# Performance work log

Hardware: AMD Instinct MI355X
Metric: run time of the kernel (lower is better)

## Reference

```python
import jax, jax.numpy as jnp
import numpy as np

PAD, BOS, EOS, UNK = 0, 1, 2, 3
B, S, V, D, L = 256, 512, 50000, 256, 128

def setup_inputs() -> dict:
    key = jax.random.key(0)
    ks = jax.random.split(key, 12)
    vocab_tensor = jax.random.randint(ks[0], (B, S), 4, V)
    parent_idx = jax.random.randint(ks[1], (B, S), 0, S)
    pbond = jax.random.randint(ks[2], (B, S), 0, 4)
    bond = jax.random.randint(ks[3], (B, S), 0, 4)
    patom = jax.random.randint(ks[4], (B, S), 0, 16)
    atom = jax.random.randint(ks[5], (B, S), 0, 16)
    btype = jax.random.randint(ks[6], (B, S), 0, 4)
    order_tensor = jnp.stack([parent_idx, pbond, bond, patom, atom, btype], axis=-1)
    lengths = jax.random.randint(ks[7], (B,), 1, S + 1)
    mask_tensor = jnp.arange(S)[None, :] < lengths[:, None]  # ragged prefix masks
    eps = jax.random.normal(ks[8], (B, L), dtype=jnp.float32)
    sc = 1.0 / np.sqrt(D)
    emb = jax.random.normal(ks[9], (V, D), dtype=jnp.float32) * sc
    Wm = jax.random.normal(ks[10], (D, L), dtype=jnp.float32) * sc
    Wv = jax.random.normal(ks[11], (D, L), dtype=jnp.float32) * sc
    Wlin = jax.random.normal(jax.random.fold_in(key, 20), (L, D), dtype=jnp.float32) / np.sqrt(L)
    Wout = jax.random.normal(jax.random.fold_in(key, 21), (D, D), dtype=jnp.float32) * sc
    return {
        'vocab_tensor': vocab_tensor, 'order_tensor': order_tensor, 'mask_tensor': mask_tensor,
        'eps': eps, 'emb': emb, 'Wm': Wm, 'bm': jnp.zeros((L,), jnp.float32),
        'Wv': Wv, 'bv': jnp.zeros((L,), jnp.float32), 'Wlin': Wlin,
        'blin': jnp.zeros((D,), jnp.float32), 'Wout': Wout, 'bout': jnp.zeros((D,), jnp.float32),
    }

def _forward(vocab_tensor, order_tensor, mask_tensor, eps, emb, Wm, bm, Wv, bv, Wlin, blin, Wout, bout):
    # --- mask bond-pos columns (torch.where assignments, vectorized) ---
    # (columns 1 and 2 set to -1 where masked; kept implicitly via vt/pad handling)
    # --- calc_chem_z path: masked vocab, parent gather, edge one-hot ---
    vt = jnp.where(mask_tensor, vocab_tensor, PAD)                      # [B,S]
    vocab_emb = emb[vt]                                                 # [B,S,D]
    oi = order_tensor[..., 0]
    oi = jnp.where(oi == -1, BOS, oi)
    parent = jnp.where(mask_tensor, jnp.take_along_axis(vt, oi, axis=1), PAD)
    parent = parent.at[:, 0].set(BOS)
    parent_emb = emb[parent]                                            # [B,S,D]
    idx = jnp.clip(order_tensor[..., 5] - 1, -1, None)
    edge_type = jnp.where((idx >= 0)[..., None],
                          jax.nn.one_hot(jnp.clip(idx, 0), 3, dtype=jnp.float32), 0.0)  # [B,S,3]
    # pooling stand-in for (undefined) StructureEncoder -> [B,D]
    m = mask_tensor[..., None].astype(jnp.float32)
    enc = ((vocab_emb + parent_emb) * m).sum(1) / jnp.maximum(m.sum(1), 1.0)
    enc = enc * (1.0 + 0.0 * edge_type.sum())  # keep edge_type in graph
    # --- LatentSampler ---
    mean = enc @ Wm + bm
    log_var = enc @ Wv + bv
    z = mean + eps * jnp.exp(0.5 * log_var)
    memory = z @ Wlin + blin                                            # [B,D]
    # --- vectorized bos/eos/pad sequence assembly (the hot loop in torch) ---
    inp = jnp.concatenate([jnp.full((B, 1), BOS, vocab_tensor.dtype), vocab_tensor], axis=1)  # [B,S+1]
    mask_ex = jnp.concatenate([jnp.ones((B, 1), bool), mask_tensor], axis=1)
    tgt = jnp.roll(inp, -1, axis=1)
    first_false = jnp.argmax(~mask_ex, axis=1)                          # first eos position
    has_false = jnp.any(~mask_ex, axis=1)
    pos = jnp.arange(S + 1)[None, :]
    tgt = jnp.where(has_false[:, None] & (pos == first_false[:, None] - 1), EOS, tgt)
    kill = has_false[:, None] & (pos >= first_false[:, None])
    tgt = jnp.where(kill, PAD, tgt)
    inp = jnp.where(kill, PAD, inp)
    # edge_index assembly (faithful, consumed by decoder in original)
    padneg = jnp.full((B, 1), -1, order_tensor.dtype)
    edge_index = jnp.concatenate([padneg, jnp.where(mask_tensor, order_tensor[..., 0], -2) + 1], axis=1)
    # --- embedding lookups + decoder stand-in + output head ---
    node_embed = emb[inp]                                               # [B,S+1,D]
    dec = node_embed + memory[:, None, :]
    dec = dec + 0.0 * edge_index[..., None].astype(jnp.float32)         # keep edge_index in graph
    word_emb = dec @ Wout + bout
    tgt_emb = emb[tgt]
    valid = (tgt != PAD)
    sq = (word_emb - tgt_emb) ** 2 * valid[..., None]
    token_loss = sq.sum() / jnp.maximum(valid.sum() * D, 1).astype(jnp.float32)
    kl = -0.5 * jnp.sum(1.0 + log_var - mean ** 2 - jnp.exp(log_var)) / B
    return token_loss, kl

def reference(vocab_tensor, order_tensor, mask_tensor, eps, emb, Wm, bm, Wv, bv, Wlin, blin, Wout, bout):
    return _forward(vocab_tensor, order_tensor, mask_tensor, eps, emb, Wm, bm, Wv, bv, Wlin, blin, Wout, bout)
```

## Files before the change

### kernel.cpp

```cpp
#include <hip/hip_runtime.h>

#define B_ 256
#define S_ 512
#define V_ 50000
#define D_ 256
#define L_ 128
#define PGRID 512

typedef __attribute__((ext_vector_type(8))) short short8;
typedef __attribute__((ext_vector_type(4))) float floatx4;

#define OFF_LENS 16
#define OFF_Q    (OFF_LENS + B_)
#define OFF_WT   (OFF_Q + B_ * D_)
#define OFF_SQP  (OFF_WT + 32768)
#define OFF_EB   (OFF_SQP + 256)
#define OFF_P    (OFF_EB + (V_ * D_ / 2))

__device__ __forceinline__ unsigned short f2bf(float x) {
    unsigned u = __float_as_uint(x);
    u += 0x7FFFu + ((u >> 16) & 1u);
    return (unsigned short)(u >> 16);
}
__device__ __forceinline__ float bf2f(unsigned short u) {
    return __uint_as_float(((unsigned)u) << 16);
}

__global__ __launch_bounds__(256) void prep_kernel(const float* __restrict__ emb,
                                                   const float* __restrict__ Wout,
                                                   unsigned short* __restrict__ embb,
                                                   unsigned short* __restrict__ Wt,
                                                   float* __restrict__ ws) {
    __shared__ float sT[64][65];
    const int tid = threadIdx.x;
    if (blockIdx.x == 0) {
        if (tid < 16) ((int*)ws)[tid] = 0;
        ws[OFF_SQP + tid] = 0.f;
    }
    if (blockIdx.x < 16) {
        const int bx = blockIdx.x;
        const int k0 = (bx & 3) * 64, n0 = (bx >> 2) * 64;
        const int c = tid & 63, rg = tid >> 6;
#pragma unroll
        for (int i = 0; i < 16; ++i) {
            int r = rg * 16 + i;
            sT[c][r] = Wout[(k0 + r) * D_ + n0 + c];
        }
        __syncthreads();
#pragma unroll
        for (int i = 0; i < 16; ++i) {
            int r = rg * 16 + i;
            Wt[(size_t)(n0 + r) * D_ + k0 + c] = f2bf(sT[r][c]);
        }
    }
    const int N4 = V_ * D_ / 4;
    for (int i = blockIdx.x * 256 + tid; i < N4; i += gridDim.x * 256) {
        float4 v = ((const float4*)emb)[i];
        ushort4 h;
        h.x = f2bf(v.x); h.y = f2bf(v.y); h.z = f2bf(v.z); h.w = f2bf(v.w);
        ((ushort4*)embb)[i] = h;
    }
}

__global__ __launch_bounds__(1024) void enclat_kernel(
    const int* __restrict__ vocab, const int* __restrict__ order,
    const int* __restrict__ mask, const unsigned short* __restrict__ embb,
    const float* __restrict__ eps,
    const float* __restrict__ Wm, const float* __restrict__ bm,
    const float* __restrict__ Wv, const float* __restrict__ bv,
    const float* __restrict__ Wlin, const float* __restrict__ blin,
    const float* __restrict__ Wout, const float* __restrict__ bout,
    int* __restrict__ lens, float* __restrict__ Q, float* __restrict__ kl_acc) {
    __shared__ int s_id1[S_], s_id2[S_];
    __shared__ float4 s_part[15 * 64];
    __shared__ float s_enc[D_];
    __shared__ float s_mean[L_], s_lv[L_], s_z[L_], s_mem[D_];
    __shared__ float s_red[256];
    __shared__ int s_cnt;
    const int b = blockIdx.x;
    const int tid = threadIdx.x;
    if (tid == 0) s_cnt = 0;
    __syncthreads();
    if (tid < S_) {
        int j = tid;
        int mk = mask[b * S_ + j];
        int id1 = 0, id2 = 0;
        if (mk) {
            id1 = vocab[b * S_ + j];
            if (j == 0) {
                id2 = 1;
            } else {
                int oi = order[(size_t)(b * S_ + j) * 6];
                if (oi == -1) oi = 1;
                id2 = mask[b * S_ + oi] ? vocab[b * S_ + oi] : 0;
            }
        }
        s_id1[j] = id1;
        s_id2[j] = id2;
        unsigned long long bal = __ballot(mk != 0);
        if ((tid & 63) == 0) atomicAdd(&s_cnt, __popcll(bal));
    }
    __syncthreads();
    const int cnt = s_cnt;
    if (tid == 0) lens[b] = cnt;
    const int jg = tid >> 6, d4 = tid & 63;
    const ushort4* eb4 = (const ushort4*)embb;
    float4 a = {0.f, 0.f, 0.f, 0.f};
#pragma unroll 4
    for (int j = jg; j < cnt; j += 16) {
        ushort4 x = eb4[(size_t)s_id1[j] * 64 + d4];
        ushort4 y = eb4[(size_t)s_id2[j] * 64 + d4];
        a.x += bf2f(x.x) + bf2f(y.x);
        a.y += bf2f(x.y) + bf2f(y.y);
        a.z += bf2f(x.z) + bf2f(y.z);
        a.w += bf2f(x.w) + bf2f(y.w);
    }
    if (jg) s_part[(jg - 1) * 64 + d4] = a;
    __syncthreads();
    if (jg == 0) {
#pragma unroll
        for (int g = 0; g < 15; ++g) {
            float4 p = s_part[g * 64 + d4];
            a.x += p.x; a.y += p.y; a.z += p.z; a.w += p.w;
        }
        float inv = 1.f / fmaxf((float)cnt, 1.f);
        a.x *= inv; a.y *= inv; a.z *= inv; a.w *= inv;
        ((float4*)s_enc)[d4] = a;
    }
    __syncthreads();
    float dot = 0.f;
    if (tid < 256) {
        const int l = tid & (L_ - 1);
        const float* W = (tid < L_) ? Wm : Wv;
        const float* bb = (tid < L_) ? bm : bv;
        dot = bb[l];
        for (int d = 0; d < D_; ++d) dot = fmaf(s_enc[d], W[d * L_ + l], dot);
        if (tid < L_) s_mean[l] = dot; else s_lv[l] = dot;
    }
    __syncthreads();
    float klp = 0.f;
    if (tid < L_) {
        float mn = s_mean[tid], lv = s_lv[tid];
        s_z[tid] = mn + eps[b * L_ + tid] * expf(0.5f * lv);
        klp = 1.f + lv - mn * mn - expf(lv);
    }
    if (tid < 256) s_red[tid] = klp;
    __syncthreads();
    for (int s = 128; s > 0; s >>= 1) {
        if (tid < s) s_red[tid] += s_red[tid + s];
        __syncthreads();
    }
    if (tid == 0) atomicAdd(kl_acc, s_red[0]);
    if (tid < 256) {
        float mem = blin[tid];
        for (int l2 = 0; l2 < L_; ++l2) mem = fmaf(s_z[l2], Wlin[l2 * D_ + tid], mem);
        s_mem[tid] = mem;
    }
    __syncthreads();
    if (tid < 256) {
        float qv = bout[tid];
        for (int k = 0; k < D_; ++k) qv = fmaf(s_mem[k], Wout[k * D_ + tid], qv);
        Q[b * D_ + tid] = qv;
    }
}

__global__ __launch_bounds__(256, 2) void pgemm_kernel(
    const unsigned short* __restrict__ embb, const unsigned short* __restrict__ Wt,
    unsigned short* __restrict__ P) {
    const int tid = threadIdx.x;
    const int wv = tid >> 6, lane = tid & 63;
    const int lo = lane & 15, hi = lane >> 4;
    const int NCH = V_ / 16;

    short8 bfr[4][8];
    const unsigned short* wbase = Wt + (size_t)(wv * 64 + lo) * D_ + hi * 8;
#pragma unroll
    for (int nt = 0; nt < 4; ++nt)
#pragma unroll
        for (int kk = 0; kk < 8; ++kk)
            bfr[nt][kk] = *(const short8*)(wbase + nt * 16 * D_ + kk * 32);

    int ch = blockIdx.x;
    const unsigned short* abase = embb + (size_t)(ch * 16 + lo) * D_ + hi * 8;
    short8 acur[8];
#pragma unroll
    for (int kk = 0; kk < 8; ++kk) acur[kk] = *(const short8*)(abase + kk * 32);

    for (; ch < NCH; ch += PGRID) {
        const int chn = (ch + PGRID < NCH) ? (ch + PGRID) : ch;
        const unsigned short* anext = embb + (size_t)(chn * 16 + lo) * D_ + hi * 8;
        short8 anxt[8];
#pragma unroll
        for (int kk = 0; kk < 8; ++kk) anxt[kk] = *(const short8*)(anext + kk * 32);

        floatx4 acc[4];
#pragma unroll
        for (int nt = 0; nt < 4; ++nt) acc[nt] = (floatx4){0.f, 0.f, 0.f, 0.f};
#pragma unroll
        for (int kk = 0; kk < 8; ++kk)
#pragma unroll
            for (int nt = 0; nt < 4; ++nt)
                acc[nt] = __builtin_amdgcn_mfma_f32_16x16x32_bf16(
                    acur[kk], bfr[nt][kk], acc[nt], 0, 0, 0);

#pragma unroll
        for (int r = 0; r < 4; ++r) {
            unsigned short* prow = P + (size_t)(ch * 16 + hi * 4 + r) * D_ + wv * 64 + lo;
#pragma unroll
            for (int nt = 0; nt < 4; ++nt) prow[nt * 16] = f2bf(acc[nt][r]);
        }
#pragma unroll
        for (int kk = 0; kk < 8; ++kk) acur[kk] = anxt[kk];
    }
}

__global__ __launch_bounds__(256) void scan_kernel(
    const int* __restrict__ vocab, const unsigned short* __restrict__ embb,
    const unsigned short* __restrict__ P, const float* __restrict__ Q,
    const int* __restrict__ lens, float* __restrict__ sqp) {
    const int tid = threadIdx.x;
    const int wv = tid >> 6, lane = tid & 63;
    const int b = blockIdx.y, chunk = blockIdx.x;
    const int len = lens[b];
    const int j0 = chunk * 32 + wv * 8;
    if (j0 > len) return;

    const int c = lane * 4;
    const float4 q4 = *(const float4*)(Q + (size_t)b * D_ + c);

    int inp[8], tgt[8];
    float wgt[8];
#pragma unroll
    for (int jj = 0; jj < 8; ++jj) {
        const int j = j0 + jj;
        const bool v = (j <= len);
        const int jc = v ? j : 0;
        inp[jj] = (jc == 0) ? 1 : vocab[b * S_ + jc - 1];
        tgt[jj] = v ? ((j < len) ? vocab[b * S_ + j] : ((len < S_) ? 2 : 1)) : 1;
        wgt[jj] = v ? 1.f : 0.f;
    }
    ushort4 pv[8], tv[8];
#pragma unroll
    for (int jj = 0; jj < 8; ++jj) {
        pv[jj] = *(const ushort4*)(P + (size_t)inp[jj] * D_ + c);
        tv[jj] = *(const ushort4*)(embb + (size_t)tgt[jj] * D_ + c);
    }
    float acc = 0.f;
#pragma unroll
    for (int jj = 0; jj < 8; ++jj) {
        float d0 = bf2f(pv[jj].x) + q4.x - bf2f(tv[jj].x);
        float d1 = bf2f(pv[jj].y) + q4.y - bf2f(tv[jj].y);
        float d2 = bf2f(pv[jj].z) + q4.z - bf2f(tv[jj].z);
        float d3 = bf2f(pv[jj].w) + q4.w - bf2f(tv[jj].w);
        float s = fmaf(d0, d0, fmaf(d1, d1, fmaf(d2, d2, d3 * d3)));
        acc = fmaf(wgt[jj], s, acc);
    }
#pragma unroll
    for (int off = 32; off; off >>= 1) acc += __shfl_down(acc, off, 64);
    if (lane == 0) atomicAdd(&sqp[(b * 4 + wv + chunk) & 255], acc);
}

__global__ __launch_bounds__(256) void finalize_kernel(const float* __restrict__ ws,
                                                       float* __restrict__ out) {
    __shared__ float s_sq[256];
    __shared__ int s_vc[256];
    const int tid = threadIdx.x;
    s_sq[tid] = ws[OFF_SQP + tid];
    s_vc[tid] = ((const int*)ws)[OFF_LENS + tid] + 1;
    __syncthreads();
    for (int s = 128; s > 0; s >>= 1) {
        if (tid < s) {
            s_sq[tid] += s_sq[tid + s];
            s_vc[tid] += s_vc[tid + s];
        }
        __syncthreads();
    }
    if (tid == 0) {
        long long denom = (long long)s_vc[0] * D_;
        if (denom < 1) denom = 1;
        out[0] = s_sq[0] / (float)denom;
        out[1] = -0.5f * ws[1] / (float)B_;
    }
}

extern "C" void kernel_launch(void* const* d_in, const int* in_sizes, int n_in,
                              void* d_out, int out_size, void* d_ws, size_t ws_size,
                              hipStream_t stream) {
    const int* vocab = (const int*)d_in[0];
    const int* order = (const int*)d_in[1];
    const int* mask  = (const int*)d_in[2];
    const float* eps  = (const float*)d_in[3];
    const float* emb  = (const float*)d_in[4];
    const float* Wm   = (const float*)d_in[5];
    const float* bm   = (const float*)d_in[6];
    const float* Wv   = (const float*)d_in[7];
    const float* bv   = (const float*)d_in[8];
    const float* Wlin = (const float*)d_in[9];
    const float* blin = (const float*)d_in[10];
    const float* Wout = (const float*)d_in[11];
    const float* bout = (const float*)d_in[12];

    float* ws = (float*)d_ws;
    int* lens = (int*)(ws + OFF_LENS);
    float* Q = ws + OFF_Q;
    unsigned short* Wt = (unsigned short*)(ws + OFF_WT);
    float* sqp = ws + OFF_SQP;
    unsigned short* embb = (unsigned short*)(ws + OFF_EB);
    unsigned short* P = (unsigned short*)(ws + OFF_P);

    prep_kernel<<<2048, 256, 0, stream>>>(emb, Wout, embb, Wt, ws);
    enclat_kernel<<<B_, 1024, 0, stream>>>(vocab, order, mask, embb, eps, Wm, bm,
                                           Wv, bv, Wlin, blin, Wout, bout,
                                           lens, Q, ws + 1);
    pgemm_kernel<<<PGRID, 256, 0, stream>>>(embb, Wt, P);
    scan_kernel<<<dim3(17, B_), 256, 0, stream>>>(vocab, embb, P, Q, lens, sqp);
    finalize_kernel<<<1, 256, 0, stream>>>(ws, (float*)d_out);
}
```

Measured before the change: 181.6 us.

## Fuse bf16 conversion into GEMM and scan/finalize into encoder kernel

The emb-to-bf16 conversion is folded into the P GEMM, which reads fp32 emb directly and writes the bf16 copy as a side output, so the separate conversion pass over the table is dropped. The per-token scan loss and the finalize step move into the per-batch encoder kernel, which uses a last-block-done atomic counter to produce the final outputs. Five launches become three and the Q/lens round trips through global memory disappear. In exchange, the GEMM loses its software prefetch of the next A tile, reads twice as many bytes per A element, and the scan work now runs with only 256 blocks.

```diff
diff --git a/kernel.cpp b/kernel.cpp
--- a/kernel.cpp
+++ b/kernel.cpp
@@ -10,11 +10,9 @@
 typedef __attribute__((ext_vector_type(8))) short short8;
 typedef __attribute__((ext_vector_type(4))) float floatx4;
 
-#define OFF_LENS 16
-#define OFF_Q    (OFF_LENS + B_)
-#define OFF_WT   (OFF_Q + B_ * D_)
-#define OFF_SQP  (OFF_WT + 32768)
-#define OFF_EB   (OFF_SQP + 256)
+#define OFF_SQP  16
+#define OFF_WT   (OFF_SQP + 256)
+#define OFF_EB   (OFF_WT + 32768)
 #define OFF_P    (OFF_EB + (V_ * D_ / 2))
 
 __device__ __forceinline__ unsigned short f2bf(float x) {
@@ -22,63 +20,114 @@
     u += 0x7FFFu + ((u >> 16) & 1u);
     return (unsigned short)(u >> 16);
 }
+__device__ __forceinline__ unsigned pk2(float a, float b) {
+    return (unsigned)f2bf(a) | ((unsigned)f2bf(b) << 16);
+}
 __device__ __forceinline__ float bf2f(unsigned short u) {
     return __uint_as_float(((unsigned)u) << 16);
 }
 
-__global__ __launch_bounds__(256) void prep_kernel(const float* __restrict__ emb,
-                                                   const float* __restrict__ Wout,
-                                                   unsigned short* __restrict__ embb,
-                                                   unsigned short* __restrict__ Wt,
-                                                   float* __restrict__ ws) {
+__global__ __launch_bounds__(256) void wt_kernel(const float* __restrict__ Wout,
+                                                 unsigned short* __restrict__ Wt,
+                                                 float* __restrict__ ws) {
     __shared__ float sT[64][65];
     const int tid = threadIdx.x;
     if (blockIdx.x == 0) {
         if (tid < 16) ((int*)ws)[tid] = 0;
         ws[OFF_SQP + tid] = 0.f;
     }
-    if (blockIdx.x < 16) {
-        const int bx = blockIdx.x;
-        const int k0 = (bx & 3) * 64, n0 = (bx >> 2) * 64;
-        const int c = tid & 63, rg = tid >> 6;
-#pragma unroll
-        for (int i = 0; i < 16; ++i) {
-            int r = rg * 16 + i;
-            sT[c][r] = Wout[(k0 + r) * D_ + n0 + c];
-        }
-        __syncthreads();
-#pragma unroll
-        for (int i = 0; i < 16; ++i) {
-            int r = rg * 16 + i;
-            Wt[(size_t)(n0 + r) * D_ + k0 + c] = f2bf(sT[r][c]);
-        }
-    }
-    const int N4 = V_ * D_ / 4;
-    for (int i = blockIdx.x * 256 + tid; i < N4; i += gridDim.x * 256) {
-        float4 v = ((const float4*)emb)[i];
-        ushort4 h;
-        h.x = f2bf(v.x); h.y = f2bf(v.y); h.z = f2bf(v.z); h.w = f2bf(v.w);
-        ((ushort4*)embb)[i] = h;
+    const int bx = blockIdx.x;
+    const int k0 = (bx & 3) * 64, n0 = (bx >> 2) * 64;
+    const int c = tid & 63, rg = tid >> 6;
+#pragma unroll
+    for (int i = 0; i < 16; ++i) {
+        int r = rg * 16 + i;
+        sT[c][r] = Wout[(k0 + r) * D_ + n0 + c];
+    }
+    __syncthreads();
+#pragma unroll
+    for (int i = 0; i < 16; ++i) {
+        int r = rg * 16 + i;
+        Wt[(size_t)(n0 + r) * D_ + k0 + c] = f2bf(sT[r][c]);
+    }
+}
+
+__global__ __launch_bounds__(256, 2) void pgemm_kernel(
+    const float* __restrict__ emb, const unsigned short* __restrict__ Wt,
+    unsigned short* __restrict__ embb, unsigned short* __restrict__ P) {
+    const int tid = threadIdx.x;
+    const int wv = tid >> 6, lane = tid & 63;
+    const int lo = lane & 15, hi = lane >> 4;
+    const int NCH = V_ / 16;
+
+    short8 bfr[4][8];
+    const unsigned short* wbase = Wt + (size_t)(wv * 64 + lo) * D_ + hi * 8;
+#pragma unroll
+    for (int nt = 0; nt < 4; ++nt)
+#pragma unroll
+        for (int kk = 0; kk < 8; ++kk)
+            bfr[nt][kk] = *(const short8*)(wbase + nt * 16 * D_ + kk * 32);
+
+    for (int ch = blockIdx.x; ch < NCH; ch += PGRID) {
+        const int row = ch * 16 + lo;
+        const float* arow = emb + (size_t)row * D_ + hi * 8;
+        short8 afr[8];
+#pragma unroll
+        for (int kk = 0; kk < 8; ++kk) {
+            float4 f0 = *(const float4*)(arow + kk * 32);
+            float4 f1 = *(const float4*)(arow + kk * 32 + 4);
+            union { unsigned u[4]; short8 s; uint4 q; } cv;
+            cv.u[0] = pk2(f0.x, f0.y);
+            cv.u[1] = pk2(f0.z, f0.w);
+            cv.u[2] = pk2(f1.x, f1.y);
+            cv.u[3] = pk2(f1.z, f1.w);
+            afr[kk] = cv.s;
+            if (wv == 0)
+                *(uint4*)(embb + (size_t)row * D_ + hi * 8 + kk * 32) = cv.q;
+        }
+
+        floatx4 acc[4];
+#pragma unroll
+        for (int nt = 0; nt < 4; ++nt) acc[nt] = (floatx4){0.f, 0.f, 0.f, 0.f};
+#pragma unroll
+        for (int kk = 0; kk < 8; ++kk)
+#pragma unroll
+            for (int nt = 0; nt < 4; ++nt)
+                acc[nt] = __builtin_amdgcn_mfma_f32_16x16x32_bf16(
+                    afr[kk], bfr[nt][kk], acc[nt], 0, 0, 0);
+
+#pragma unroll
+        for (int r = 0; r < 4; ++r) {
+            unsigned short* prow = P + (size_t)(ch * 16 + hi * 4 + r) * D_ + wv * 64 + lo;
+#pragma unroll
+            for (int nt = 0; nt < 4; ++nt) prow[nt * 16] = f2bf(acc[nt][r]);
+        }
     }
 }
 
 __global__ __launch_bounds__(1024) void enclat_kernel(
     const int* __restrict__ vocab, const int* __restrict__ order,
     const int* __restrict__ mask, const unsigned short* __restrict__ embb,
-    const float* __restrict__ eps,
+    const unsigned short* __restrict__ P, const float* __restrict__ eps,
     const float* __restrict__ Wm, const float* __restrict__ bm,
     const float* __restrict__ Wv, const float* __restrict__ bv,
     const float* __restrict__ Wlin, const float* __restrict__ blin,
     const float* __restrict__ Wout, const float* __restrict__ bout,
-    int* __restrict__ lens, float* __restrict__ Q, float* __restrict__ kl_acc) {
+    float* __restrict__ ws, float* __restrict__ out) {
     __shared__ int s_id1[S_], s_id2[S_];
     __shared__ float4 s_part[15 * 64];
     __shared__ float s_enc[D_];
-    __shared__ float s_mean[L_], s_lv[L_], s_z[L_], s_mem[D_];
+    __shared__ float s_mean[L_], s_lv[L_], s_z[L_], s_mem[D_], s_Q[D_];
     __shared__ float s_red[256];
-    __shared__ int s_cnt;
+    __shared__ float s_wred[16];
+    __shared__ int s_cnt, s_prev;
     const int b = blockIdx.x;
     const int tid = threadIdx.x;
+    float* kl_acc = ws + 1;
+    int* vc_acc = (int*)ws + 2;
+    int* done = (int*)ws + 3;
+    float* sqp = ws + OFF_SQP;
+
     if (tid == 0) s_cnt = 0;
     __syncthreads();
     if (tid < S_) {
@@ -102,7 +151,6 @@
     }
     __syncthreads();
     const int cnt = s_cnt;
-    if (tid == 0) lens[b] = cnt;
     const int jg = tid >> 6, d4 = tid & 63;
     const ushort4* eb4 = (const ushort4*)embb;
     float4 a = {0.f, 0.f, 0.f, 0.f};
@@ -150,7 +198,7 @@
         if (tid < s) s_red[tid] += s_red[tid + s];
         __syncthreads();
     }
-    if (tid == 0) atomicAdd(kl_acc, s_red[0]);
+    const float kl_part = s_red[0];
     if (tid < 256) {
         float mem = blin[tid];
         for (int l2 = 0; l2 < L_; ++l2) mem = fmaf(s_z[l2], Wlin[l2 * D_ + tid], mem);
@@ -160,126 +208,55 @@
     if (tid < 256) {
         float qv = bout[tid];
         for (int k = 0; k < D_; ++k) qv = fmaf(s_mem[k], Wout[k * D_ + tid], qv);
-        Q[b * D_ + tid] = qv;
-    }
-}
-
-__global__ __launch_bounds__(256, 2) void pgemm_kernel(
-    const unsigned short* __restrict__ embb, const unsigned short* __restrict__ Wt,
-    unsigned short* __restrict__ P) {
-    const int tid = threadIdx.x;
-    const int wv = tid >> 6, lane = tid & 63;
-    const int lo = lane & 15, hi = lane >> 4;
-    const int NCH = V_ / 16;
-
-    short8 bfr[4][8];
-    const unsigned short* wbase = Wt + (size_t)(wv * 64 + lo) * D_ + hi * 8;
-#pragma unroll
-    for (int nt = 0; nt < 4; ++nt)
-#pragma unroll
-        for (int kk = 0; kk < 8; ++kk)
-            bfr[nt][kk] = *(const short8*)(wbase + nt * 16 * D_ + kk * 32);
-
-    int ch = blockIdx.x;
-    const unsigned short* abase = embb + (size_t)(ch * 16 + lo) * D_ + hi * 8;
-    short8 acur[8];
-#pragma unroll
-    for (int kk = 0; kk < 8; ++kk) acur[kk] = *(const short8*)(abase + kk * 32);
-
-    for (; ch < NCH; ch += PGRID) {
-        const int chn = (ch + PGRID < NCH) ? (ch + PGRID) : ch;
-        const unsigned short* anext = embb + (size_t)(chn * 16 + lo) * D_ + hi * 8;
-        short8 anxt[8];
-#pragma unroll
-        for (int kk = 0; kk < 8; ++kk) anxt[kk] = *(const short8*)(anext + kk * 32);
-
-        floatx4 acc[4];
-#pragma unroll
-        for (int nt = 0; nt < 4; ++nt) acc[nt] = (floatx4){0.f, 0.f, 0.f, 0.f};
-#pragma unroll
-        for (int kk = 0; kk < 8; ++kk)
-#pragma unroll
-            for (int nt = 0; nt < 4; ++nt)
-                acc[nt] = __builtin_amdgcn_mfma_f32_16x16x32_bf16(
-                    acur[kk], bfr[nt][kk], acc[nt], 0, 0, 0);
-
-#pragma unroll
-        for (int r = 0; r < 4; ++r) {
-            unsigned short* prow = P + (size_t)(ch * 16 + hi * 4 + r) * D_ + wv * 64 + lo;
-#pragma unroll
-            for (int nt = 0; nt < 4; ++nt) prow[nt * 16] = f2bf(acc[nt][r]);
-        }
-#pragma unroll
-        for (int kk = 0; kk < 8; ++kk) acur[kk] = anxt[kk];
-    }
-}
-
-__global__ __launch_bounds__(256) void scan_kernel(
-    const int* __restrict__ vocab, const unsigned short* __restrict__ embb,
-    const unsigned short* __restrict__ P, const float* __restrict__ Q,
-    const int* __restrict__ lens, float* __restrict__ sqp) {
-    const int tid = threadIdx.x;
-    const int wv = tid >> 6, lane = tid & 63;
-    const int b = blockIdx.y, chunk = blockIdx.x;
-    const int len = lens[b];
-    const int j0 = chunk * 32 + wv * 8;
-    if (j0 > len) return;
-
+        s_Q[tid] = qv;
+    }
+    __syncthreads();
+    const int lane = tid & 63;
     const int c = lane * 4;
-    const float4 q4 = *(const float4*)(Q + (size_t)b * D_ + c);
-
-    int inp[8], tgt[8];
-    float wgt[8];
-#pragma unroll
-    for (int jj = 0; jj < 8; ++jj) {
-        const int j = j0 + jj;
-        const bool v = (j <= len);
-        const int jc = v ? j : 0;
-        inp[jj] = (jc == 0) ? 1 : vocab[b * S_ + jc - 1];
-        tgt[jj] = v ? ((j < len) ? vocab[b * S_ + j] : ((len < S_) ? 2 : 1)) : 1;
-        wgt[jj] = v ? 1.f : 0.f;
-    }
-    ushort4 pv[8], tv[8];
-#pragma unroll
-    for (int jj = 0; jj < 8; ++jj) {
-        pv[jj] = *(const ushort4*)(P + (size_t)inp[jj] * D_ + c);
-        tv[jj] = *(const ushort4*)(embb + (size_t)tgt[jj] * D_ + c);
-    }
+    const float4 q4 = *(const float4*)(s_Q + c);
     float acc = 0.f;
-#pragma unroll
-    for (int jj = 0; jj < 8; ++jj) {
-        float d0 = bf2f(pv[jj].x) + q4.x - bf2f(tv[jj].x);
-        float d1 = bf2f(pv[jj].y) + q4.y - bf2f(tv[jj].y);
-        float d2 = bf2f(pv[jj].z) + q4.z - bf2f(tv[jj].z);
-        float d3 = bf2f(pv[jj].w) + q4.w - bf2f(tv[jj].w);
-        float s = fmaf(d0, d0, fmaf(d1, d1, fmaf(d2, d2, d3 * d3)));
-        acc = fmaf(wgt[jj], s, acc);
+    for (int j = jg; j <= cnt; j += 16) {
+        const int inp = (j == 0) ? 1 : s_id1[j - 1];
+        const int tgt = (j < cnt) ? s_id1[j] : ((cnt < S_) ? 2 : 1);
+        const ushort4 pv = *(const ushort4*)(P + (size_t)inp * D_ + c);
+        const ushort4 tv = *(const ushort4*)(embb + (size_t)tgt * D_ + c);
+        float d0 = bf2f(pv.x) + q4.x - bf2f(tv.x);
+        float d1 = bf2f(pv.y) + q4.y - bf2f(tv.y);
+        float d2 = bf2f(pv.z) + q4.z - bf2f(tv.z);
+        float d3 = bf2f(pv.w) + q4.w - bf2f(tv.w);
+        acc += fmaf(d0, d0, fmaf(d1, d1, fmaf(d2, d2, d3 * d3)));
     }
 #pragma unroll
     for (int off = 32; off; off >>= 1) acc += __shfl_down(acc, off, 64);
-    if (lane == 0) atomicAdd(&sqp[(b * 4 + wv + chunk) & 255], acc);
-}
-
-__global__ __launch_bounds__(256) void finalize_kernel(const float* __restrict__ ws,
-                                                       float* __restrict__ out) {
-    __shared__ float s_sq[256];
-    __shared__ int s_vc[256];
-    const int tid = threadIdx.x;
-    s_sq[tid] = ws[OFF_SQP + tid];
-    s_vc[tid] = ((const int*)ws)[OFF_LENS + tid] + 1;
-    __syncthreads();
-    for (int s = 128; s > 0; s >>= 1) {
-        if (tid < s) {
-            s_sq[tid] += s_sq[tid + s];
-            s_vc[tid] += s_vc[tid + s];
-        }
+    if (lane == 0) s_wred[jg] = acc;
+    __syncthreads();
+    if (tid == 0) {
+        float tot = 0.f;
+#pragma unroll
+        for (int g = 0; g < 16; ++g) tot += s_wred[g];
+        sqp[b] = tot;
+        atomicAdd(kl_acc, kl_part);
+        atomicAdd(vc_acc, cnt + 1);
+        __threadfence();
+        s_prev = atomicAdd(done, 1);
+    }
+    __syncthreads();
+    if (s_prev == B_ - 1) {
+        float v = (tid < 256) ? atomicAdd(&sqp[tid], 0.f) : 0.f;
+        if (tid < 256) s_red[tid] = v;
         __syncthreads();
-    }
-    if (tid == 0) {
-        long long denom = (long long)s_vc[0] * D_;
-        if (denom < 1) denom = 1;
-        out[0] = s_sq[0] / (float)denom;
-        out[1] = -0.5f * ws[1] / (float)B_;
+        for (int s = 128; s > 0; s >>= 1) {
+            if (tid < s) s_red[tid] += s_red[tid + s];
+            __syncthreads();
+        }
+        if (tid == 0) {
+            float kl = atomicAdd(kl_acc, 0.f);
+            int vc = atomicAdd(vc_acc, 0);
+            long long denom = (long long)vc * D_;
+            if (denom < 1) denom = 1;
+            out[0] = s_red[0] / (float)denom;
+            out[1] = -0.5f * kl / (float)B_;
+        }
     }
 }
 
@@ -301,18 +278,13 @@
     const float* bout = (const float*)d_in[12];
 
     float* ws = (float*)d_ws;
-    int* lens = (int*)(ws + OFF_LENS);
-    float* Q = ws + OFF_Q;
     unsigned short* Wt = (unsigned short*)(ws + OFF_WT);
-    float* sqp = ws + OFF_SQP;
     unsigned short* embb = (unsigned short*)(ws + OFF_EB);
     unsigned short* P = (unsigned short*)(ws + OFF_P);
 
-    prep_kernel<<<2048, 256, 0, stream>>>(emb, Wout, embb, Wt, ws);
-    enclat_kernel<<<B_, 1024, 0, stream>>>(vocab, order, mask, embb, eps, Wm, bm,
-                                           Wv, bv, Wlin, blin, Wout, bout,
-                                           lens, Q, ws + 1);
-    pgemm_kernel<<<PGRID, 256, 0, stream>>>(embb, Wt, P);
-    scan_kernel<<<dim3(17, B_), 256, 0, stream>>>(vocab, embb, P, Q, lens, sqp);
-    finalize_kernel<<<1, 256, 0, stream>>>(ws, (float*)d_out);
-}
+    wt_kernel<<<16, 256, 0, stream>>>(Wout, Wt, ws);
+    pgemm_kernel<<<PGRID, 256, 0, stream>>>(emb, Wt, embb, P);
+    enclat_kernel<<<B_, 1024, 0, stream>>>(vocab, order, mask, embb, P, eps,
+                                           Wm, bm, Wv, bv, Wlin, blin, Wout, bout,
+                                           ws, (float*)d_out);
+}
```

After: 194.8 us. +7.2%, slower.

## Split encoder gather across more blocks and fold finalize into scan

Applied to the files above, without the earlier changes.

The single per-batch encoder/latent kernel is split in two. A gather kernel spreads each batch row's embedding sum over eight blocks and writes partial sums, and a smaller latent kernel reduces those partials and computes mean, log-variance, z, memory and Q. The finalize kernel is removed: the last scan block, detected with an atomic completion counter, does the final reduction and writes both losses. The aim is better GPU occupancy for the latency-bound gather and one fewer kernel launch. The cost is an extra round trip of partial sums through global memory and reliance on the workspace counters being zeroed.

```diff
diff --git a/kernel.cpp b/kernel.cpp
--- a/kernel.cpp
+++ b/kernel.cpp
@@ -10,11 +10,12 @@
 typedef __attribute__((ext_vector_type(8))) short short8;
 typedef __attribute__((ext_vector_type(4))) float floatx4;
 
-#define OFF_LENS 16
-#define OFF_Q    (OFF_LENS + B_)
+#define OFF_SQP  16
+#define OFF_LENS 272
+#define OFF_Q    528
 #define OFF_WT   (OFF_Q + B_ * D_)
-#define OFF_SQP  (OFF_WT + 32768)
-#define OFF_EB   (OFF_SQP + 256)
+#define OFF_EP   (OFF_WT + 32768)
+#define OFF_EB   (OFF_EP + B_ * 8 * D_)
 #define OFF_P    (OFF_EB + (V_ * D_ / 2))
 
 __device__ __forceinline__ unsigned short f2bf(float x) {
@@ -62,17 +63,105 @@
     }
 }
 
-__global__ __launch_bounds__(1024) void enclat_kernel(
+__global__ __launch_bounds__(256, 2) void pgemm_kernel(
+    const unsigned short* __restrict__ embb, const unsigned short* __restrict__ Wt,
+    unsigned short* __restrict__ P) {
+    const int tid = threadIdx.x;
+    const int wv = tid >> 6, lane = tid & 63;
+    const int lo = lane & 15, hi = lane >> 4;
+    const int NCH = V_ / 16;
+
+    short8 bfr[4][8];
+    const unsigned short* wbase = Wt + (size_t)(wv * 64 + lo) * D_ + hi * 8;
+#pragma unroll
+    for (int nt = 0; nt < 4; ++nt)
+#pragma unroll
+        for (int kk = 0; kk < 8; ++kk)
+            bfr[nt][kk] = *(const short8*)(wbase + nt * 16 * D_ + kk * 32);
+
+    int ch = blockIdx.x;
+    const unsigned short* abase = embb + (size_t)(ch * 16 + lo) * D_ + hi * 8;
+    short8 acur[8];
+#pragma unroll
+    for (int kk = 0; kk < 8; ++kk) acur[kk] = *(const short8*)(abase + kk * 32);
+
+    for (; ch < NCH; ch += PGRID) {
+        const int chn = (ch + PGRID < NCH) ? (ch + PGRID) : ch;
+        const unsigned short* anext = embb + (size_t)(chn * 16 + lo) * D_ + hi * 8;
+        short8 anxt[8];
+#pragma unroll
+        for (int kk = 0; kk < 8; ++kk) anxt[kk] = *(const short8*)(anext + kk * 32);
+
+        floatx4 acc[4];
+#pragma unroll
+        for (int nt = 0; nt < 4; ++nt) acc[nt] = (floatx4){0.f, 0.f, 0.f, 0.f};
+#pragma unroll
+        for (int kk = 0; kk < 8; ++kk)
+#pragma unroll
+            for (int nt = 0; nt < 4; ++nt)
+                acc[nt] = __builtin_amdgcn_mfma_f32_16x16x32_bf16(
+                    acur[kk], bfr[nt][kk], acc[nt], 0, 0, 0);
+
+#pragma unroll
+        for (int r = 0; r < 4; ++r) {
+            unsigned short* prow = P + (size_t)(ch * 16 + hi * 4 + r) * D_ + wv * 64 + lo;
+#pragma unroll
+            for (int nt = 0; nt < 4; ++nt) prow[nt * 16] = f2bf(acc[nt][r]);
+        }
+#pragma unroll
+        for (int kk = 0; kk < 8; ++kk) acur[kk] = anxt[kk];
+    }
+}
+
+__global__ __launch_bounds__(256) void gather_kernel(
     const int* __restrict__ vocab, const int* __restrict__ order,
     const int* __restrict__ mask, const unsigned short* __restrict__ embb,
+    float* __restrict__ enc_part) {
+    const int b = blockIdx.x >> 3, o = blockIdx.x & 7;
+    const int tid = threadIdx.x;
+    const int jg = tid >> 6, lane = tid & 63;
+    const ushort4* eb4 = (const ushort4*)embb;
+    float4 a = {0.f, 0.f, 0.f, 0.f};
+    for (int j = o + 8 * jg; j < S_; j += 32) {
+        if (!mask[b * S_ + j]) break;
+        int id1 = vocab[b * S_ + j];
+        int id2;
+        if (j == 0) {
+            id2 = 1;
+        } else {
+            int oi = order[(size_t)(b * S_ + j) * 6];
+            if (oi == -1) oi = 1;
+            id2 = mask[b * S_ + oi] ? vocab[b * S_ + oi] : 0;
+        }
+        ushort4 x = eb4[(size_t)id1 * 64 + lane];
+        ushort4 y = eb4[(size_t)id2 * 64 + lane];
+        a.x += bf2f(x.x) + bf2f(y.x);
+        a.y += bf2f(x.y) + bf2f(y.y);
+        a.z += bf2f(x.z) + bf2f(y.z);
+        a.w += bf2f(x.w) + bf2f(y.w);
+    }
+    __shared__ float4 sp[3][64];
+    if (jg) sp[jg - 1][lane] = a;
+    __syncthreads();
+    if (jg == 0) {
+#pragma unroll
+        for (int g = 0; g < 3; ++g) {
+            float4 p = sp[g][lane];
+            a.x += p.x; a.y += p.y; a.z += p.z; a.w += p.w;
+        }
+        *(float4*)(enc_part + (size_t)blockIdx.x * D_ + 4 * lane) = a;
+    }
+}
+
+__global__ __launch_bounds__(256) void latent_kernel(
+    const int* __restrict__ mask, const float* __restrict__ enc_part,
     const float* __restrict__ eps,
     const float* __restrict__ Wm, const float* __restrict__ bm,
     const float* __restrict__ Wv, const float* __restrict__ bv,
     const float* __restrict__ Wlin, const float* __restrict__ blin,
     const float* __restrict__ Wout, const float* __restrict__ bout,
-    int* __restrict__ lens, float* __restrict__ Q, float* __restrict__ kl_acc) {
-    __shared__ int s_id1[S_], s_id2[S_];
-    __shared__ float4 s_part[15 * 64];
+    int* __restrict__ lens, float* __restrict__ Q,
+    float* __restrict__ kl_acc, int* __restrict__ vc_acc) {
     __shared__ float s_enc[D_];
     __shared__ float s_mean[L_], s_lv[L_], s_z[L_], s_mem[D_];
     __shared__ float s_red[256];
@@ -81,59 +170,24 @@
     const int tid = threadIdx.x;
     if (tid == 0) s_cnt = 0;
     __syncthreads();
-    if (tid < S_) {
-        int j = tid;
-        int mk = mask[b * S_ + j];
-        int id1 = 0, id2 = 0;
-        if (mk) {
-            id1 = vocab[b * S_ + j];
-            if (j == 0) {
-                id2 = 1;
-            } else {
-                int oi = order[(size_t)(b * S_ + j) * 6];
-                if (oi == -1) oi = 1;
-                id2 = mask[b * S_ + oi] ? vocab[b * S_ + oi] : 0;
-            }
-        }
-        s_id1[j] = id1;
-        s_id2[j] = id2;
-        unsigned long long bal = __ballot(mk != 0);
-        if ((tid & 63) == 0) atomicAdd(&s_cnt, __popcll(bal));
+    {
+        int m0 = mask[b * S_ + tid] != 0;
+        int m1 = mask[b * S_ + 256 + tid] != 0;
+        unsigned long long b0 = __ballot(m0), b1 = __ballot(m1);
+        if ((tid & 63) == 0) atomicAdd(&s_cnt, __popcll(b0) + __popcll(b1));
     }
     __syncthreads();
     const int cnt = s_cnt;
-    if (tid == 0) lens[b] = cnt;
-    const int jg = tid >> 6, d4 = tid & 63;
-    const ushort4* eb4 = (const ushort4*)embb;
-    float4 a = {0.f, 0.f, 0.f, 0.f};
-#pragma unroll 4
-    for (int j = jg; j < cnt; j += 16) {
-        ushort4 x = eb4[(size_t)s_id1[j] * 64 + d4];
-        ushort4 y = eb4[(size_t)s_id2[j] * 64 + d4];
-        a.x += bf2f(x.x) + bf2f(y.x);
-        a.y += bf2f(x.y) + bf2f(y.y);
-        a.z += bf2f(x.z) + bf2f(y.z);
-        a.w += bf2f(x.w) + bf2f(y.w);
-    }
-    if (jg) s_part[(jg - 1) * 64 + d4] = a;
-    __syncthreads();
-    if (jg == 0) {
-#pragma unroll
-        for (int g = 0; g < 15; ++g) {
-            float4 p = s_part[g * 64 + d4];
-            a.x += p.x; a.y += p.y; a.z += p.z; a.w += p.w;
-        }
-        float inv = 1.f / fmaxf((float)cnt, 1.f);
-        a.x *= inv; a.y *= inv; a.z *= inv; a.w *= inv;
-        ((float4*)s_enc)[d4] = a;
-    }
-    __syncthreads();
-    float dot = 0.f;
-    if (tid < 256) {
+    float e = 0.f;
+#pragma unroll
+    for (int o = 0; o < 8; ++o) e += enc_part[((size_t)(b * 8 + o)) * D_ + tid];
+    s_enc[tid] = e / fmaxf((float)cnt, 1.f);
+    __syncthreads();
+    {
         const int l = tid & (L_ - 1);
         const float* W = (tid < L_) ? Wm : Wv;
         const float* bb = (tid < L_) ? bm : bv;
-        dot = bb[l];
+        float dot = bb[l];
         for (int d = 0; d < D_; ++d) dot = fmaf(s_enc[d], W[d * L_ + l], dot);
         if (tid < L_) s_mean[l] = dot; else s_lv[l] = dot;
     }
@@ -144,142 +198,100 @@
         s_z[tid] = mn + eps[b * L_ + tid] * expf(0.5f * lv);
         klp = 1.f + lv - mn * mn - expf(lv);
     }
-    if (tid < 256) s_red[tid] = klp;
+    s_red[tid] = klp;
     __syncthreads();
     for (int s = 128; s > 0; s >>= 1) {
         if (tid < s) s_red[tid] += s_red[tid + s];
         __syncthreads();
     }
-    if (tid == 0) atomicAdd(kl_acc, s_red[0]);
-    if (tid < 256) {
-        float mem = blin[tid];
-        for (int l2 = 0; l2 < L_; ++l2) mem = fmaf(s_z[l2], Wlin[l2 * D_ + tid], mem);
-        s_mem[tid] = mem;
-    }
-    __syncthreads();
-    if (tid < 256) {
-        float qv = bout[tid];
-        for (int k = 0; k < D_; ++k) qv = fmaf(s_mem[k], Wout[k * D_ + tid], qv);
-        Q[b * D_ + tid] = qv;
-    }
-}
-
-__global__ __launch_bounds__(256, 2) void pgemm_kernel(
-    const unsigned short* __restrict__ embb, const unsigned short* __restrict__ Wt,
-    unsigned short* __restrict__ P) {
-    const int tid = threadIdx.x;
-    const int wv = tid >> 6, lane = tid & 63;
-    const int lo = lane & 15, hi = lane >> 4;
-    const int NCH = V_ / 16;
-
-    short8 bfr[4][8];
-    const unsigned short* wbase = Wt + (size_t)(wv * 64 + lo) * D_ + hi * 8;
-#pragma unroll
-    for (int nt = 0; nt < 4; ++nt)
-#pragma unroll
-        for (int kk = 0; kk < 8; ++kk)
-            bfr[nt][kk] = *(const short8*)(wbase + nt * 16 * D_ + kk * 32);
-
-    int ch = blockIdx.x;
-    const unsigned short* abase = embb + (size_t)(ch * 16 + lo) * D_ + hi * 8;
-    short8 acur[8];
-#pragma unroll
-    for (int kk = 0; kk < 8; ++kk) acur[kk] = *(const short8*)(abase + kk * 32);
-
-    for (; ch < NCH; ch += PGRID) {
-        const int chn = (ch + PGRID < NCH) ? (ch + PGRID) : ch;
-        const unsigned short* anext = embb + (size_t)(chn * 16 + lo) * D_ + hi * 8;
-        short8 anxt[8];
-#pragma unroll
-        for (int kk = 0; kk < 8; ++kk) anxt[kk] = *(const short8*)(anext + kk * 32);
-
-        floatx4 acc[4];
-#pragma unroll
-        for (int nt = 0; nt < 4; ++nt) acc[nt] = (floatx4){0.f, 0.f, 0.f, 0.f};
-#pragma unroll
-        for (int kk = 0; kk < 8; ++kk)
-#pragma unroll
-            for (int nt = 0; nt < 4; ++nt)
-                acc[nt] = __builtin_amdgcn_mfma_f32_16x16x32_bf16(
-                    acur[kk], bfr[nt][kk], acc[nt], 0, 0, 0);
-
-#pragma unroll
-        for (int r = 0; r < 4; ++r) {
-            unsigned short* prow = P + (size_t)(ch * 16 + hi * 4 + r) * D_ + wv * 64 + lo;
-#pragma unroll
-            for (int nt = 0; nt < 4; ++nt) prow[nt * 16] = f2bf(acc[nt][r]);
-        }
-#pragma unroll
-        for (int kk = 0; kk < 8; ++kk) acur[kk] = anxt[kk];
-    }
-}
-
+    if (tid == 0) {
+        atomicAdd(kl_acc, s_red[0]);
+        atomicAdd(vc_acc, cnt + 1);
+        lens[b] = cnt;
+    }
+    float mem = blin[tid];
+    for (int l2 = 0; l2 < L_; ++l2) mem = fmaf(s_z[l2], Wlin[l2 * D_ + tid], mem);
+    s_mem[tid] = mem;
+    __syncthreads();
+    float qv = bout[tid];
+    for (int k = 0; k < D_; ++k) qv = fmaf(s_mem[k], Wout[k * D_ + tid], qv);
+    Q[b * D_ + tid] = qv;
+}
+
+#define NBLK (17 * B_)
 __global__ __launch_bounds__(256) void scan_kernel(
     const int* __restrict__ vocab, const unsigned short* __restrict__ embb,
     const unsigned short* __restrict__ P, const float* __restrict__ Q,
-    const int* __restrict__ lens, float* __restrict__ sqp) {
+    const int* __restrict__ lens, float* __restrict__ ws,
+    float* __restrict__ out) {
+    __shared__ float s_red[256];
+    __shared__ int s_prev;
     const int tid = threadIdx.x;
     const int wv = tid >> 6, lane = tid & 63;
     const int b = blockIdx.y, chunk = blockIdx.x;
     const int len = lens[b];
     const int j0 = chunk * 32 + wv * 8;
-    if (j0 > len) return;
-
-    const int c = lane * 4;
-    const float4 q4 = *(const float4*)(Q + (size_t)b * D_ + c);
-
-    int inp[8], tgt[8];
-    float wgt[8];
-#pragma unroll
-    for (int jj = 0; jj < 8; ++jj) {
-        const int j = j0 + jj;
-        const bool v = (j <= len);
-        const int jc = v ? j : 0;
-        inp[jj] = (jc == 0) ? 1 : vocab[b * S_ + jc - 1];
-        tgt[jj] = v ? ((j < len) ? vocab[b * S_ + j] : ((len < S_) ? 2 : 1)) : 1;
-        wgt[jj] = v ? 1.f : 0.f;
-    }
-    ushort4 pv[8], tv[8];
-#pragma unroll
-    for (int jj = 0; jj < 8; ++jj) {
-        pv[jj] = *(const ushort4*)(P + (size_t)inp[jj] * D_ + c);
-        tv[jj] = *(const ushort4*)(embb + (size_t)tgt[jj] * D_ + c);
-    }
-    float acc = 0.f;
-#pragma unroll
-    for (int jj = 0; jj < 8; ++jj) {
-        float d0 = bf2f(pv[jj].x) + q4.x - bf2f(tv[jj].x);
-        float d1 = bf2f(pv[jj].y) + q4.y - bf2f(tv[jj].y);
-        float d2 = bf2f(pv[jj].z) + q4.z - bf2f(tv[jj].z);
-        float d3 = bf2f(pv[jj].w) + q4.w - bf2f(tv[jj].w);
-        float s = fmaf(d0, d0, fmaf(d1, d1, fmaf(d2, d2, d3 * d3)));
-        acc = fmaf(wgt[jj], s, acc);
-    }
-#pragma unroll
-    for (int off = 32; off; off >>= 1) acc += __shfl_down(acc, off, 64);
-    if (lane == 0) atomicAdd(&sqp[(b * 4 + wv + chunk) & 255], acc);
-}
-
-__global__ __launch_bounds__(256) void finalize_kernel(const float* __restrict__ ws,
-                                                       float* __restrict__ out) {
-    __shared__ float s_sq[256];
-    __shared__ int s_vc[256];
-    const int tid = threadIdx.x;
-    s_sq[tid] = ws[OFF_SQP + tid];
-    s_vc[tid] = ((const int*)ws)[OFF_LENS + tid] + 1;
-    __syncthreads();
-    for (int s = 128; s > 0; s >>= 1) {
-        if (tid < s) {
-            s_sq[tid] += s_sq[tid + s];
-            s_vc[tid] += s_vc[tid + s];
-        }
+    float* kl_acc = ws + 1;
+    int* vc_acc = (int*)ws + 2;
+    int* done = (int*)ws + 3;
+    float* sqp = ws + OFF_SQP;
+
+    if (j0 <= len) {
+        const int c = lane * 4;
+        const float4 q4 = *(const float4*)(Q + (size_t)b * D_ + c);
+        int inp[8], tgt[8];
+        float wgt[8];
+#pragma unroll
+        for (int jj = 0; jj < 8; ++jj) {
+            const int j = j0 + jj;
+            const bool v = (j <= len);
+            const int jc = v ? j : 0;
+            inp[jj] = (jc == 0) ? 1 : vocab[b * S_ + jc - 1];
+            tgt[jj] = v ? ((j < len) ? vocab[b * S_ + j] : ((len < S_) ? 2 : 1)) : 1;
+            wgt[jj] = v ? 1.f : 0.f;
+        }
+        ushort4 pv[8], tv[8];
+#pragma unroll
+        for (int jj = 0; jj < 8; ++jj) {
+            pv[jj] = *(const ushort4*)(P + (size_t)inp[jj] * D_ + c);
+            tv[jj] = *(const ushort4*)(embb + (size_t)tgt[jj] * D_ + c);
+        }
+        float acc = 0.f;
+#pragma unroll
+        for (int jj = 0; jj < 8; ++jj) {
+            float d0 = bf2f(pv[jj].x) + q4.x - bf2f(tv[jj].x);
+            float d1 = bf2f(pv[jj].y) + q4.y - bf2f(tv[jj].y);
+            float d2 = bf2f(pv[jj].z) + q4.z - bf2f(tv[jj].z);
+            float d3 = bf2f(pv[jj].w) + q4.w - bf2f(tv[jj].w);
+            float s = fmaf(d0, d0, fmaf(d1, d1, fmaf(d2, d2, d3 * d3)));
+            acc = fmaf(wgt[jj], s, acc);
+        }
+#pragma unroll
+        for (int off = 32; off; off >>= 1) acc += __shfl_down(acc, off, 64);
+        if (lane == 0) atomicAdd(&sqp[(b * 4 + wv + chunk) & 255], acc);
+    }
+    __syncthreads();
+    if (tid == 0) {
+        __threadfence();
+        s_prev = atomicAdd(done, 1);
+    }
+    __syncthreads();
+    if (s_prev == NBLK - 1) {
+        float v = atomicAdd(&sqp[tid], 0.f);
+        s_red[tid] = v;
         __syncthreads();
-    }
-    if (tid == 0) {
-        long long denom = (long long)s_vc[0] * D_;
-        if (denom < 1) denom = 1;
-        out[0] = s_sq[0] / (float)denom;
-        out[1] = -0.5f * ws[1] / (float)B_;
+        for (int s = 128; s > 0; s >>= 1) {
+            if (tid < s) s_red[tid] += s_red[tid + s];
+            __syncthreads();
+        }
+        if (tid == 0) {
+            float kl = atomicAdd(kl_acc, 0.f);
+            int vc = atomicAdd(vc_acc, 0);
+            long long denom = (long long)vc * D_;
+            if (denom < 1) denom = 1;
+            out[0] = s_red[0] / (float)denom;
+            out[1] = -0.5f * kl / (float)B_;
+        }
     }
 }
 
@@ -304,15 +316,16 @@
     int* lens = (int*)(ws + OFF_LENS);
     float* Q = ws + OFF_Q;
     unsigned short* Wt = (unsigned short*)(ws + OFF_WT);
-    float* sqp = ws + OFF_SQP;
+    float* enc_part = ws + OFF_EP;
     unsigned short* embb = (unsigned short*)(ws + OFF_EB);
     unsigned short* P = (unsigned short*)(ws + OFF_P);
 
     prep_kernel<<<2048, 256, 0, stream>>>(emb, Wout, embb, Wt, ws);
-    enclat_kernel<<<B_, 1024, 0, stream>>>(vocab, order, mask, embb, eps, Wm, bm,
-                                           Wv, bv, Wlin, blin, Wout, bout,
-                                           lens, Q, ws + 1);
     pgemm_kernel<<<PGRID, 256, 0, stream>>>(embb, Wt, P);
-    scan_kernel<<<dim3(17, B_), 256, 0, stream>>>(vocab, embb, P, Q, lens, sqp);
-    finalize_kernel<<<1, 256, 0, stream>>>(ws, (float*)d_out);
-}
+    gather_kernel<<<B_ * 8, 256, 0, stream>>>(vocab, order, mask, embb, enc_part);
+    latent_kernel<<<B_, 256, 0, stream>>>(mask, enc_part, eps, Wm, bm, Wv, bv,
+                                          Wlin, blin, Wout, bout, lens, Q,
+                                          ws + 1, (int*)ws + 2);
+    scan_kernel<<<dim3(17, B_), 256, 0, stream>>>(vocab, embb, P, Q, lens, ws,
+                                                  (float*)d_out);
+}
```

Result: slower. 322.9 us (+77.8%).
